# Optimization experiments

Hardware: AMD Instinct MI355X
Metric: run time of the kernel (lower is better)

## Reference

```python
import jax, jax.numpy as jnp
import numpy as np

N_NODES = 100000
N_EDGES = 800000
IN_FEATS = 256
N_HIDDEN = 256
N_CLASSES = 64


def setup_inputs() -> dict:
    key = jax.random.key(0)
    ks = jax.random.split(key, 10)
    def lin(k, fi, fo):
        # Xavier-ish scale like nn.Linear init
        return jax.random.normal(k, (fi, fo), dtype=jnp.float32) / np.sqrt(fi)
    return {
        "x": jax.random.normal(ks[0], (N_NODES, IN_FEATS), dtype=jnp.float32),
        "src": jax.random.randint(ks[1], (N_EDGES,), 0, N_NODES, dtype=jnp.int32),
        "dst": jax.random.randint(ks[2], (N_EDGES,), 0, N_NODES, dtype=jnp.int32),
        "W_self1": lin(ks[3], IN_FEATS, N_HIDDEN),
        "W_neigh1": lin(ks[4], IN_FEATS, N_HIDDEN),
        "b1": jnp.zeros((N_HIDDEN,), jnp.float32),
        "W_self2": lin(ks[5], N_HIDDEN, N_HIDDEN),
        "W_neigh2": lin(ks[6], N_HIDDEN, N_HIDDEN),
        "b2": jnp.zeros((N_HIDDEN,), jnp.float32),
        "W_self3": lin(ks[7], N_HIDDEN, N_CLASSES),
        "W_neigh3": lin(ks[8], N_HIDDEN, N_CLASSES),
        "b3": jnp.zeros((N_CLASSES,), jnp.float32),
    }


def _sage_conv(h, src, dst, inv_deg, W_self, W_neigh, b):
    # mean-aggregate in-neighbor (src) features at dst nodes
    agg = jax.ops.segment_sum(h[src], dst, num_segments=N_NODES)  # [N, d]
    agg = agg * inv_deg[:, None]
    # DGL SAGEConv(mean): fc_self(h_dst) + fc_neigh(h_neigh) + bias
    return h @ W_self + agg @ W_neigh + b


def reference(x, src, dst, W_self1, W_neigh1, b1, W_self2, W_neigh2, b2,
              W_self3, W_neigh3, b3):
    deg = jax.ops.segment_sum(jnp.ones_like(dst, dtype=x.dtype), dst,
                              num_segments=N_NODES)
    inv_deg = 1.0 / jnp.maximum(deg, 1.0)  # DGL clamps in-degree at 1
    h = _sage_conv(x, src, dst, inv_deg, W_self1, W_neigh1, b1)
    h = jax.nn.relu(h)  # dropout is identity at inference
    h = _sage_conv(h, src, dst, inv_deg, W_self2, W_neigh2, b2)
    h = jax.nn.relu(h)
    h = _sage_conv(h, src, dst, inv_deg, W_self3, W_neigh3, b3)
    return h
```

## Files before the change

kernel.cpp:

```cpp
#include <hip/hip_runtime.h>


#define NN 100000
#define NE 800000
#define MPAD 100096

typedef __attribute__((ext_vector_type(8))) short short8;
typedef __attribute__((ext_vector_type(4))) float floatx4;

__device__ __forceinline__ float bf2f(unsigned short u) {
    unsigned int x = ((unsigned int)u) << 16;
    return __builtin_bit_cast(float, x);
}
__device__ __forceinline__ unsigned short f2bf(float f) {
    unsigned int x = __builtin_bit_cast(unsigned int, f);
    x += 0x7fffu + ((x >> 16) & 1u);
    return (unsigned short)(x >> 16);
}

__device__ __forceinline__ void gl_lds16(const unsigned short* g, unsigned short* l) {
    __builtin_amdgcn_global_load_lds(
        (const __attribute__((address_space(1))) unsigned int*)g,
        (__attribute__((address_space(3))) unsigned int*)l,
        16, 0, 0);
}

__global__ void degi_kernel(const int* __restrict__ dst, int* __restrict__ deg) {
    int e = blockIdx.x * blockDim.x + threadIdx.x;
    if (e < NE) atomicAdd(&deg[dst[e]], 1);
}

__global__ __launch_bounds__(1024) void scan_kernel(const int4* __restrict__ deg4,
                                                    int4* __restrict__ cur4) {
    __shared__ int wsum[16];
    __shared__ int carry_s;
    const int tid = threadIdx.x, lane = tid & 63, w = tid >> 6;
    if (tid == 0) carry_s = 0;
    __syncthreads();
    for (int base = 0; base < 25600; base += 1024) {
        int i = base + tid;
        int4 v = deg4[i];
        int t = v.x + v.y + v.z + v.w;
        int s = t;
        #pragma unroll
        for (int off = 1; off < 64; off <<= 1) {
            int u = __shfl_up(s, off, 64);
            if (lane >= off) s += u;
        }
        if (lane == 63) wsum[w] = s;
        __syncthreads();
        if (w == 0) {
            int ws_ = (lane < 16) ? wsum[lane] : 0;
            int t2 = ws_;
            #pragma unroll
            for (int off = 1; off < 16; off <<= 1) {
                int u = __shfl_up(t2, off, 64);
                if (lane >= off) t2 += u;
            }
            if (lane < 16) wsum[lane] = t2 - ws_;
        }
        __syncthreads();
        int excl = carry_s + wsum[w] + (s - t);
        int4 o;
        o.x = excl; o.y = o.x + v.x; o.z = o.y + v.y; o.w = o.z + v.z;
        cur4[i] = o;
        __syncthreads();
        if (tid == 1023) carry_s = excl + t;
        __syncthreads();
    }
}

__global__ void scatter_kernel(const int* __restrict__ src, const int* __restrict__ dst,
                               int* __restrict__ cursor, int* __restrict__ nbr) {
    int e = blockIdx.x * blockDim.x + threadIdx.x;
    if (e < NE) {
        int pos = atomicAdd(&cursor[dst[e]], 1);
        nbr[pos] = src[e];
    }
}

__global__ void cast_x_kernel(const float4* __restrict__ x, unsigned short* __restrict__ H) {
    int gid = blockIdx.x * 256 + threadIdx.x;
    if (gid >= NN * 64) return;
    int row = gid >> 6, col = (gid & 63) * 4;
    float4 v = x[gid];
    ushort4 o;
    o.x = f2bf(v.x); o.y = f2bf(v.y); o.z = f2bf(v.z); o.w = f2bf(v.w);
    *(ushort4*)&H[(size_t)row * 512 + col] = o;
}

__global__ void wprep_kernel(const float* __restrict__ Ws, const float* __restrict__ Wn,
                             unsigned short* __restrict__ Bt) {
    int idx = blockIdx.x * 256 + threadIdx.x;
    if (idx >= 256 * 512) return;
    int n = idx >> 9, k = idx & 511;
    float v = (k < 256) ? Ws[(size_t)k * 256 + n] : Wn[(size_t)(k - 256) * 256 + n];
    Bt[idx] = f2bf(v);
}

__global__ void wprep3_kernel(const float* __restrict__ Ws3, const float* __restrict__ Wn3,
                              const float* __restrict__ b3, unsigned short* __restrict__ Bt3,
                              float* __restrict__ b3ext) {
    int idx = blockIdx.x * 256 + threadIdx.x;
    if (idx < 128 * 256) {
        int n = idx >> 8, k = idx & 255;
        float v = (n < 64) ? Ws3[(size_t)k * 64 + n] : Wn3[(size_t)k * 64 + (n - 64)];
        Bt3[idx] = f2bf(v);
    }
    if (idx < 128) b3ext[idx] = (idx < 64) ? b3[idx] : 0.f;
}

__global__ __launch_bounds__(256) void gather_bf16(unsigned short* __restrict__ H,
                                                   const int* __restrict__ nbr,
                                                   const int* __restrict__ cursor,
                                                   const int* __restrict__ deg) {
    __shared__ int sidx[4][64];
    const int lane = threadIdx.x & 63;
    const int sub  = threadIdx.x >> 6;
    const int d = blockIdx.x * 4 + sub;
    if (d >= NN) return;
    const int dg = deg[d];
    const int end = cursor[d];
    const int start = end - dg;
    const int co = lane * 4;
    const int dgc = (dg < 64) ? dg : 64;

    if (lane < dgc) sidx[sub][lane] = nbr[start + lane];
    const int* si = sidx[sub];

    float acc[4] = {0.f, 0.f, 0.f, 0.f};

    int r = 0;
    for (; r + 8 <= dgc; r += 8) {
        int s0 = si[r + 0], s1 = si[r + 1], s2 = si[r + 2], s3 = si[r + 3];
        int s4 = si[r + 4], s5 = si[r + 5], s6 = si[r + 6], s7 = si[r + 7];
        ushort4 v0 = *(const ushort4*)&H[(size_t)s0 * 512 + co];
        ushort4 v1 = *(const ushort4*)&H[(size_t)s1 * 512 + co];
        ushort4 v2 = *(const ushort4*)&H[(size_t)s2 * 512 + co];
        ushort4 v3 = *(const ushort4*)&H[(size_t)s3 * 512 + co];
        ushort4 v4 = *(const ushort4*)&H[(size_t)s4 * 512 + co];
        ushort4 v5 = *(const ushort4*)&H[(size_t)s5 * 512 + co];
        ushort4 v6 = *(const ushort4*)&H[(size_t)s6 * 512 + co];
        ushort4 v7 = *(const ushort4*)&H[(size_t)s7 * 512 + co];
        acc[0] += (bf2f(v0.x) + bf2f(v1.x)) + (bf2f(v2.x) + bf2f(v3.x))
                + (bf2f(v4.x) + bf2f(v5.x)) + (bf2f(v6.x) + bf2f(v7.x));
        acc[1] += (bf2f(v0.y) + bf2f(v1.y)) + (bf2f(v2.y) + bf2f(v3.y))
                + (bf2f(v4.y) + bf2f(v5.y)) + (bf2f(v6.y) + bf2f(v7.y));
        acc[2] += (bf2f(v0.z) + bf2f(v1.z)) + (bf2f(v2.z) + bf2f(v3.z))
                + (bf2f(v4.z) + bf2f(v5.z)) + (bf2f(v6.z) + bf2f(v7.z));
        acc[3] += (bf2f(v0.w) + bf2f(v1.w)) + (bf2f(v2.w) + bf2f(v3.w))
                + (bf2f(v4.w) + bf2f(v5.w)) + (bf2f(v6.w) + bf2f(v7.w));
    }
    for (; r + 4 <= dgc; r += 4) {
        int s0 = si[r + 0], s1 = si[r + 1], s2 = si[r + 2], s3 = si[r + 3];
        ushort4 v0 = *(const ushort4*)&H[(size_t)s0 * 512 + co];
        ushort4 v1 = *(const ushort4*)&H[(size_t)s1 * 512 + co];
        ushort4 v2 = *(const ushort4*)&H[(size_t)s2 * 512 + co];
        ushort4 v3 = *(const ushort4*)&H[(size_t)s3 * 512 + co];
        acc[0] += (bf2f(v0.x) + bf2f(v1.x)) + (bf2f(v2.x) + bf2f(v3.x));
        acc[1] += (bf2f(v0.y) + bf2f(v1.y)) + (bf2f(v2.y) + bf2f(v3.y));
        acc[2] += (bf2f(v0.z) + bf2f(v1.z)) + (bf2f(v2.z) + bf2f(v3.z));
        acc[3] += (bf2f(v0.w) + bf2f(v1.w)) + (bf2f(v2.w) + bf2f(v3.w));
    }
    for (; r < dgc; ++r) {
        int s0 = si[r];
        ushort4 v0 = *(const ushort4*)&H[(size_t)s0 * 512 + co];
        acc[0] += bf2f(v0.x); acc[1] += bf2f(v0.y);
        acc[2] += bf2f(v0.z); acc[3] += bf2f(v0.w);
    }
    for (int j = start + 64; j < end; ++j) {
        int s0 = nbr[j];
        ushort4 v0 = *(const ushort4*)&H[(size_t)s0 * 512 + co];
        acc[0] += bf2f(v0.x); acc[1] += bf2f(v0.y);
        acc[2] += bf2f(v0.z); acc[3] += bf2f(v0.w);
    }

    const float inv = 1.0f / fmaxf((float)dg, 1.0f);
    ushort4 o;
    o.x = f2bf(acc[0] * inv); o.y = f2bf(acc[1] * inv);
    o.z = f2bf(acc[2] * inv); o.w = f2bf(acc[3] * inv);
    *(ushort4*)&H[(size_t)d * 512 + 256 + co] = o;
}

template <int KT, bool RELU>
__global__ __launch_bounds__(256, 2) void sage_mfma(const unsigned short* __restrict__ A,
                                                    const unsigned short* __restrict__ Bt,
                                                    const float* __restrict__ bias,
                                                    unsigned short* __restrict__ Cout, int ldc) {
    __shared__ unsigned short sm[2][2][128 * 64];
    constexpr int BSTR = KT * 64;
    const int tid = threadIdx.x;
    const int lane = tid & 63;
    const int w = tid >> 6, wm = w >> 1, wn = w & 1;
    const int m0 = blockIdx.x * 128, n0 = blockIdx.y * 128;
    const int lr = lane & 15, lq = lane >> 4;

    const int srow = w * 32 + (lane >> 3);
    const int scol = (lane & 7) * 8;
    const unsigned short* gA = A  + (size_t)(m0 + srow) * 512  + scol;
    const unsigned short* gB = Bt + (size_t)(n0 + srow) * BSTR + scol;

    floatx4 acc[4][4] = {};

    {
        unsigned short* lA = &sm[0][0][(w * 32) * 64];
        unsigned short* lB = &sm[0][1][(w * 32) * 64];
        #pragma unroll
        for (int c = 0; c < 4; ++c) {
            gl_lds16(gA + (size_t)c * 8 * 512,  lA + c * 8 * 64);
            gl_lds16(gB + (size_t)c * 8 * BSTR, lB + c * 8 * 64);
        }
    }
    __syncthreads();

    #pragma unroll
    for (int t = 0; t < KT; ++t) {
        const int buf = t & 1;
        if (t + 1 < KT) {
            unsigned short* lA = &sm[buf ^ 1][0][(w * 32) * 64];
            unsigned short* lB = &sm[buf ^ 1][1][(w * 32) * 64];
            const unsigned short* pA = gA + (size_t)(t + 1) * 64;
            const unsigned short* pB = gB + (size_t)(t + 1) * 64;
            #pragma unroll
            for (int c = 0; c < 4; ++c) {
                gl_lds16(pA + (size_t)c * 8 * 512,  lA + c * 8 * 64);
                gl_lds16(pB + (size_t)c * 8 * BSTR, lB + c * 8 * 64);
            }
        }
        const unsigned short* bA = &sm[buf][0][0];
        const unsigned short* bB = &sm[buf][1][0];
        #pragma unroll
        for (int ks = 0; ks < 2; ++ks) {
            short8 af[4], bf[4];
            #pragma unroll
            for (int mi = 0; mi < 4; ++mi)
                af[mi] = *(const short8*)&bA[(wm * 64 + mi * 16 + lr) * 64 + ks * 32 + lq * 8];
            #pragma unroll
            for (int ni = 0; ni < 4; ++ni)
                bf[ni] = *(const short8*)&bB[(wn * 64 + ni * 16 + lr) * 64 + ks * 32 + lq * 8];
            #pragma unroll
            for (int mi = 0; mi < 4; ++mi)
                #pragma unroll
                for (int ni = 0; ni < 4; ++ni)
                    acc[mi][ni] = __builtin_amdgcn_mfma_f32_16x16x32_bf16(bf[ni], af[mi],
                                                                          acc[mi][ni], 0, 0, 0);
        }
        __syncthreads();
    }

    unsigned short* slab = &sm[0][0][0];
    #pragma unroll
    for (int mi = 0; mi < 4; ++mi) {
        const int rl = wm * 64 + mi * 16 + lr;
        #pragma unroll
        for (int ni = 0; ni < 4; ++ni) {
            const int cl = wn * 64 + ni * 16 + lq * 4;
            const float4 bv = *(const float4*)&bias[n0 + cl];
            float v0 = acc[mi][ni][0] + bv.x;
            float v1 = acc[mi][ni][1] + bv.y;
            float v2 = acc[mi][ni][2] + bv.z;
            float v3 = acc[mi][ni][3] + bv.w;
            if (RELU) {
                v0 = fmaxf(v0, 0.f); v1 = fmaxf(v1, 0.f);
                v2 = fmaxf(v2, 0.f); v3 = fmaxf(v3, 0.f);
            }
            ushort4 o;
            o.x = f2bf(v0); o.y = f2bf(v1); o.z = f2bf(v2); o.w = f2bf(v3);
            *(ushort4*)&slab[rl * 136 + cl] = o;
        }
    }
    __syncthreads();
    #pragma unroll
    for (int it = 0; it < 8; ++it) {
        int idx = it * 256 + tid;
        int row = idx >> 4, c8 = (idx & 15) * 8;
        if (m0 + row < NN) {
            short8 v = *(const short8*)&slab[row * 136 + c8];
            *(short8*)&Cout[(size_t)(m0 + row) * ldc + n0 + c8] = v;
        }
    }
}

__global__ __launch_bounds__(256) void final_out(const unsigned short* __restrict__ T,
                                                 const int* __restrict__ nbr,
                                                 const int* __restrict__ cursor,
                                                 const int* __restrict__ deg,
                                                 float* __restrict__ out) {
    __shared__ int sidx[4][64];
    const int lane = threadIdx.x & 63;
    const int sub  = threadIdx.x >> 6;
    const int d = blockIdx.x * 4 + sub;
    if (d >= NN) return;
    const int g  = lane >> 4;
    const int li = lane & 15;
    const int dg = deg[d];
    const int end = cursor[d];
    const int start = end - dg;
    const int co = li * 4;
    const int dgc = (dg < 64) ? dg : 64;

    ushort4 sv = *(const ushort4*)&T[(size_t)d * 128 + co];

    if (lane < dgc) sidx[sub][lane] = nbr[start + lane];
    const int* si = sidx[sub];

    float acc[4] = {0.f, 0.f, 0.f, 0.f};
    int r = g;
    for (; r + 4 < dgc; r += 8) {
        int s0 = si[r], s1 = si[r + 4];
        ushort4 v0 = *(const ushort4*)&T[(size_t)s0 * 128 + 64 + co];
        ushort4 v1 = *(const ushort4*)&T[(size_t)s1 * 128 + 64 + co];
        acc[0] += bf2f(v0.x) + bf2f(v1.x);
        acc[1] += bf2f(v0.y) + bf2f(v1.y);
        acc[2] += bf2f(v0.z) + bf2f(v1.z);
        acc[3] += bf2f(v0.w) + bf2f(v1.w);
    }
    for (; r < dgc; r += 4) {
        int s0 = si[r];
        ushort4 v0 = *(const ushort4*)&T[(size_t)s0 * 128 + 64 + co];
        acc[0] += bf2f(v0.x); acc[1] += bf2f(v0.y);
        acc[2] += bf2f(v0.z); acc[3] += bf2f(v0.w);
    }
    for (int j = start + 64 + g; j < end; j += 4) {
        int s0 = nbr[j];
        ushort4 v0 = *(const ushort4*)&T[(size_t)s0 * 128 + 64 + co];
        acc[0] += bf2f(v0.x); acc[1] += bf2f(v0.y);
        acc[2] += bf2f(v0.z); acc[3] += bf2f(v0.w);
    }

    #pragma unroll
    for (int i = 0; i < 4; ++i) {
        acc[i] += __shfl_xor(acc[i], 16, 64);
        acc[i] += __shfl_xor(acc[i], 32, 64);
    }

    if (g == 0) {
        const float inv = 1.0f / fmaxf((float)dg, 1.0f);
        float4 o;
        o.x = bf2f(sv.x) + acc[0] * inv;
        o.y = bf2f(sv.y) + acc[1] * inv;
        o.z = bf2f(sv.z) + acc[2] * inv;
        o.w = bf2f(sv.w) + acc[3] * inv;
        *(float4*)&out[(size_t)d * 64 + co] = o;
    }
}

extern "C" void kernel_launch(void* const* d_in, const int* in_sizes, int n_in,
                              void* d_out, int out_size, void* d_ws, size_t ws_size,
                              hipStream_t stream) {
    const float* x   = (const float*)d_in[0];
    const int*   src = (const int*)d_in[1];
    const int*   dst = (const int*)d_in[2];
    const float* Ws1 = (const float*)d_in[3];
    const float* Wn1 = (const float*)d_in[4];
    const float* b1  = (const float*)d_in[5];
    const float* Ws2 = (const float*)d_in[6];
    const float* Wn2 = (const float*)d_in[7];
    const float* b2  = (const float*)d_in[8];
    const float* Ws3 = (const float*)d_in[9];
    const float* Wn3 = (const float*)d_in[10];
    const float* b3  = (const float*)d_in[11];

    unsigned short* H1  = (unsigned short*)d_ws;
    unsigned short* H2  = H1  + (size_t)MPAD * 512;
    unsigned short* T   = H2  + (size_t)MPAD * 512;
    unsigned short* Bt1 = T   + (size_t)MPAD * 128;
    unsigned short* Bt2 = Bt1 + 256 * 512;
    unsigned short* Bt3 = Bt2 + 256 * 512;
    float* b3ext = (float*)(Bt3 + 128 * 256);
    int* deg    = (int*)(b3ext + 128);
    int* cursor = deg + 102400;
    int* nbr    = cursor + 102400;

    hipMemsetAsync(deg, 0, 102400 * sizeof(int), stream);
    degi_kernel<<<(NE + 255) / 256, 256, 0, stream>>>(dst, deg);
    scan_kernel<<<1, 1024, 0, stream>>>((const int4*)deg, (int4*)cursor);
    scatter_kernel<<<(NE + 255) / 256, 256, 0, stream>>>(src, dst, cursor, nbr);

    cast_x_kernel<<<(NN * 64 + 255) / 256, 256, 0, stream>>>((const float4*)x, H1);
    wprep_kernel<<<512, 256, 0, stream>>>(Ws1, Wn1, Bt1);
    wprep_kernel<<<512, 256, 0, stream>>>(Ws2, Wn2, Bt2);
    wprep3_kernel<<<128, 256, 0, stream>>>(Ws3, Wn3, b3, Bt3, b3ext);

    const int gatherBlocks = (NN + 3) / 4;
    const dim3 g2(MPAD / 128, 2), g1(MPAD / 128, 1);

    gather_bf16<<<gatherBlocks, 256, 0, stream>>>(H1, nbr, cursor, deg);
    sage_mfma<8, true><<<g2, 256, 0, stream>>>(H1, Bt1, b1, H2, 512);

    gather_bf16<<<gatherBlocks, 256, 0, stream>>>(H2, nbr, cursor, deg);
    sage_mfma<8, true><<<g2, 256, 0, stream>>>(H2, Bt2, b2, H1, 512);

    sage_mfma<4, false><<<g1, 256, 0, stream>>>(H1, Bt3, b3ext, T, 128);
    final_out<<<gatherBlocks, 256, 0, stream>>>(T, nbr, cursor, deg, (float*)d_out);
}
```

Before: 559.7 us.

## Parallelize degree scan and shrink GEMM K-tile with swizzled LDS for occupancy

Replaces the single-block serial prefix scan over node degrees with a three-kernel multi-block scan (per-block scan, block-sum scan, add-back). The GEMM kernel halves its K tile from 64 to 32, cutting LDS per block to about 34KB. It also adds an XOR swizzle on LDS columns to reduce bank conflicts, and raises the launch-bounds occupancy hint from 2 to 4 blocks per CU. The trade-off is twice as many K iterations and barriers per tile, plus two extra kernel launches for the scan.

```diff
diff --git a/kernel.cpp b/kernel.cpp
--- a/kernel.cpp
+++ b/kernel.cpp
@@ -30,44 +30,59 @@
     if (e < NE) atomicAdd(&deg[dst[e]], 1);
 }
 
-__global__ __launch_bounds__(1024) void scan_kernel(const int4* __restrict__ deg4,
-                                                    int4* __restrict__ cur4) {
-    __shared__ int wsum[16];
-    __shared__ int carry_s;
+__global__ __launch_bounds__(256) void scan1(const int4* __restrict__ deg4,
+                                             int4* __restrict__ cur4,
+                                             int* __restrict__ bsum) {
+    __shared__ int woff[4];
     const int tid = threadIdx.x, lane = tid & 63, w = tid >> 6;
-    if (tid == 0) carry_s = 0;
+    const int i = blockIdx.x * 256 + tid;
+    int4 v = deg4[i];
+    int t = v.x + v.y + v.z + v.w;
+    int s = t;
+    #pragma unroll
+    for (int off = 1; off < 64; off <<= 1) {
+        int u = __shfl_up(s, off, 64);
+        if (lane >= off) s += u;
+    }
+    if (lane == 63) woff[w] = s;
     __syncthreads();
-    for (int base = 0; base < 25600; base += 1024) {
-        int i = base + tid;
-        int4 v = deg4[i];
-        int t = v.x + v.y + v.z + v.w;
-        int s = t;
+    if (tid == 0) {
+        int a0 = woff[0], a1 = woff[1], a2 = woff[2], a3 = woff[3];
+        woff[0] = 0; woff[1] = a0; woff[2] = a0 + a1; woff[3] = a0 + a1 + a2;
+        bsum[blockIdx.x] = a0 + a1 + a2 + a3;
+    }
+    __syncthreads();
+    int excl = woff[w] + (s - t);
+    int4 o;
+    o.x = excl; o.y = o.x + v.x; o.z = o.y + v.y; o.w = o.z + v.z;
+    cur4[i] = o;
+}
+
+__global__ void scan2(int* __restrict__ bsum) {
+    const int lane = threadIdx.x;
+    int carry = 0;
+    for (int base = 0; base < 100; base += 64) {
+        int n = 100 - base; if (n > 64) n = 64;
+        int v = (lane < n) ? bsum[base + lane] : 0;
+        int s = v;
         #pragma unroll
         for (int off = 1; off < 64; off <<= 1) {
             int u = __shfl_up(s, off, 64);
             if (lane >= off) s += u;
         }
-        if (lane == 63) wsum[w] = s;
-        __syncthreads();
-        if (w == 0) {
-            int ws_ = (lane < 16) ? wsum[lane] : 0;
-            int t2 = ws_;
-            #pragma unroll
-            for (int off = 1; off < 16; off <<= 1) {
-                int u = __shfl_up(t2, off, 64);
-                if (lane >= off) t2 += u;
-            }
-            if (lane < 16) wsum[lane] = t2 - ws_;
-        }
-        __syncthreads();
-        int excl = carry_s + wsum[w] + (s - t);
-        int4 o;
-        o.x = excl; o.y = o.x + v.x; o.z = o.y + v.y; o.w = o.z + v.z;
-        cur4[i] = o;
-        __syncthreads();
-        if (tid == 1023) carry_s = excl + t;
-        __syncthreads();
-    }
+        int tot = __shfl(s, 63, 64);
+        if (lane < n) bsum[base + lane] = carry + s - v;
+        carry += tot;
+    }
+}
+
+__global__ __launch_bounds__(256) void scan3(int4* __restrict__ cur4,
+                                             const int* __restrict__ bsum) {
+    const int i = blockIdx.x * 256 + threadIdx.x;
+    const int o = bsum[blockIdx.x];
+    int4 v = cur4[i];
+    v.x += o; v.y += o; v.z += o; v.w += o;
+    cur4[i] = v;
 }
 
 __global__ void scatter_kernel(const int* __restrict__ src, const int* __restrict__ dst,
@@ -183,32 +198,34 @@
 }
 
 template <int KT, bool RELU>
-__global__ __launch_bounds__(256, 2) void sage_mfma(const unsigned short* __restrict__ A,
+__global__ __launch_bounds__(256, 4) void sage_mfma(const unsigned short* __restrict__ A,
                                                     const unsigned short* __restrict__ Bt,
                                                     const float* __restrict__ bias,
                                                     unsigned short* __restrict__ Cout, int ldc) {
-    __shared__ unsigned short sm[2][2][128 * 64];
-    constexpr int BSTR = KT * 64;
+    __shared__ unsigned short lds[17408];
+    constexpr int BSTR = KT * 32;
     const int tid = threadIdx.x;
     const int lane = tid & 63;
     const int w = tid >> 6, wm = w >> 1, wn = w & 1;
     const int m0 = blockIdx.x * 128, n0 = blockIdx.y * 128;
     const int lr = lane & 15, lq = lane >> 4;
 
-    const int srow = w * 32 + (lane >> 3);
-    const int scol = (lane & 7) * 8;
-    const unsigned short* gA = A  + (size_t)(m0 + srow) * 512  + scol;
-    const unsigned short* gB = Bt + (size_t)(n0 + srow) * BSTR + scol;
+    const int sr   = lane >> 2;
+    const int ssl  = (lane & 3) ^ (sr & 3);
+    const unsigned short* gA = A  + (size_t)(m0 + w * 32 + sr) * 512  + ssl * 8;
+    const unsigned short* gB = Bt + (size_t)(n0 + w * 32 + sr) * BSTR + ssl * 8;
+
+    const int lqx = (lq ^ (lr & 3)) * 8;
 
     floatx4 acc[4][4] = {};
 
     {
-        unsigned short* lA = &sm[0][0][(w * 32) * 64];
-        unsigned short* lB = &sm[0][1][(w * 32) * 64];
-        #pragma unroll
-        for (int c = 0; c < 4; ++c) {
-            gl_lds16(gA + (size_t)c * 8 * 512,  lA + c * 8 * 64);
-            gl_lds16(gB + (size_t)c * 8 * BSTR, lB + c * 8 * 64);
+        unsigned short* lA = &lds[0 * 8192 + (w * 32) * 32];
+        unsigned short* lB = &lds[0 * 8192 + 4096 + (w * 32) * 32];
+        #pragma unroll
+        for (int c = 0; c < 2; ++c) {
+            gl_lds16(gA + (size_t)c * 16 * 512,  lA + c * 512);
+            gl_lds16(gB + (size_t)c * 16 * BSTR, lB + c * 512);
         }
     }
     __syncthreads();
@@ -217,38 +234,35 @@
     for (int t = 0; t < KT; ++t) {
         const int buf = t & 1;
         if (t + 1 < KT) {
-            unsigned short* lA = &sm[buf ^ 1][0][(w * 32) * 64];
-            unsigned short* lB = &sm[buf ^ 1][1][(w * 32) * 64];
-            const unsigned short* pA = gA + (size_t)(t + 1) * 64;
-            const unsigned short* pB = gB + (size_t)(t + 1) * 64;
+            unsigned short* lA = &lds[(buf ^ 1) * 8192 + (w * 32) * 32];
+            unsigned short* lB = &lds[(buf ^ 1) * 8192 + 4096 + (w * 32) * 32];
+            const unsigned short* pA = gA + (size_t)(t + 1) * 32;
+            const unsigned short* pB = gB + (size_t)(t + 1) * 32;
             #pragma unroll
-            for (int c = 0; c < 4; ++c) {
-                gl_lds16(pA + (size_t)c * 8 * 512,  lA + c * 8 * 64);
-                gl_lds16(pB + (size_t)c * 8 * BSTR, lB + c * 8 * 64);
+            for (int c = 0; c < 2; ++c) {
+                gl_lds16(pA + (size_t)c * 16 * 512,  lA + c * 512);
+                gl_lds16(pB + (size_t)c * 16 * BSTR, lB + c * 512);
             }
         }
-        const unsigned short* bA = &sm[buf][0][0];
-        const unsigned short* bB = &sm[buf][1][0];
-        #pragma unroll
-        for (int ks = 0; ks < 2; ++ks) {
-            short8 af[4], bf[4];
-            #pragma unroll
-            for (int mi = 0; mi < 4; ++mi)
-                af[mi] = *(const short8*)&bA[(wm * 64 + mi * 16 + lr) * 64 + ks * 32 + lq * 8];
+        const unsigned short* bA = &lds[buf * 8192];
+        const unsigned short* bB = bA + 4096;
+        short8 af[4], bf[4];
+        #pragma unroll
+        for (int mi = 0; mi < 4; ++mi)
+            af[mi] = *(const short8*)&bA[(wm * 64 + mi * 16 + lr) * 32 + lqx];
+        #pragma unroll
+        for (int ni = 0; ni < 4; ++ni)
+            bf[ni] = *(const short8*)&bB[(wn * 64 + ni * 16 + lr) * 32 + lqx];
+        #pragma unroll
+        for (int mi = 0; mi < 4; ++mi)
             #pragma unroll
             for (int ni = 0; ni < 4; ++ni)
-                bf[ni] = *(const short8*)&bB[(wn * 64 + ni * 16 + lr) * 64 + ks * 32 + lq * 8];
-            #pragma unroll
-            for (int mi = 0; mi < 4; ++mi)
-                #pragma unroll
-                for (int ni = 0; ni < 4; ++ni)
-                    acc[mi][ni] = __builtin_amdgcn_mfma_f32_16x16x32_bf16(bf[ni], af[mi],
-                                                                          acc[mi][ni], 0, 0, 0);
-        }
+                acc[mi][ni] = __builtin_amdgcn_mfma_f32_16x16x32_bf16(bf[ni], af[mi],
+                                                                      acc[mi][ni], 0, 0, 0);
         __syncthreads();
     }
 
-    unsigned short* slab = &sm[0][0][0];
+    unsigned short* slab = &lds[0];
     #pragma unroll
     for (int mi = 0; mi < 4; ++mi) {
         const int rl = wm * 64 + mi * 16 + lr;
@@ -371,10 +385,13 @@
     int* deg    = (int*)(b3ext + 128);
     int* cursor = deg + 102400;
     int* nbr    = cursor + 102400;
+    int* bsum   = nbr + NE;
 
     hipMemsetAsync(deg, 0, 102400 * sizeof(int), stream);
     degi_kernel<<<(NE + 255) / 256, 256, 0, stream>>>(dst, deg);
-    scan_kernel<<<1, 1024, 0, stream>>>((const int4*)deg, (int4*)cursor);
+    scan1<<<100, 256, 0, stream>>>((const int4*)deg, (int4*)cursor, bsum);
+    scan2<<<1, 64, 0, stream>>>(bsum);
+    scan3<<<100, 256, 0, stream>>>((int4*)cursor, bsum);
     scatter_kernel<<<(NE + 255) / 256, 256, 0, stream>>>(src, dst, cursor, nbr);
 
     cast_x_kernel<<<(NN * 64 + 255) / 256, 256, 0, stream>>>((const float4*)x, H1);
@@ -386,11 +403,11 @@
     const dim3 g2(MPAD / 128, 2), g1(MPAD / 128, 1);
 
     gather_bf16<<<gatherBlocks, 256, 0, stream>>>(H1, nbr, cursor, deg);
-    sage_mfma<8, true><<<g2, 256, 0, stream>>>(H1, Bt1, b1, H2, 512);
+    sage_mfma<16, true><<<g2, 256, 0, stream>>>(H1, Bt1, b1, H2, 512);
 
     gather_bf16<<<gatherBlocks, 256, 0, stream>>>(H2, nbr, cursor, deg);
-    sage_mfma<8, true><<<g2, 256, 0, stream>>>(H2, Bt2, b2, H1, 512);
-
-    sage_mfma<4, false><<<g1, 256, 0, stream>>>(H1, Bt3, b3ext, T, 128);
+    sage_mfma<16, true><<<g2, 256, 0, stream>>>(H2, Bt2, b2, H1, 512);
+
+    sage_mfma<8, false><<<g1, 256, 0, stream>>>(H1, Bt3, b3ext, T, 128);
     final_out<<<gatherBlocks, 256, 0, stream>>>(T, nbr, cursor, deg, (float*)d_out);
 }
```

New measurement: 533.3 us. 1.05x faster.
